# Performance work log

Measured on AMD Instinct MI355X. Metric: run time of the kernel, lower is better.

## Reference

```python
import jax, jax.numpy as jnp
import numpy as np

B = 1024
S_OUT, S_IN, D_IN = 30, 17, 3
H = 4
DKQ_I, DV_I, HID_I, OUT_I = 6, 8, 256, 64
DKQ_O, DV_O, HID_O = 64, 64, 1024
OUT_O = 36 * S_OUT  # 1080


def _mha(x, wq, bq, wk, bk, wv, bv, dkq):
    """Vectorized multi-head self-attention over all heads at once.
    x: [..., P, d_in]; wq/wk: [H, d_in, dkq]; wv: [H, d_in, dv].
    Returns context [..., H, P, dv] (matches torch stack+permute ordering)."""
    q = jnp.einsum('...pd,hdk->...hpk', x, wq) + bq[:, None, :]
    k = jnp.einsum('...pd,hdk->...hpk', x, wk) + bk[:, None, :]
    v = jnp.einsum('...pd,hdv->...hpv', x, wv) + bv[:, None, :]
    scores = jnp.einsum('...hpk,...hqk->...hpq', q, k) / jnp.sqrt(jnp.asarray(dkq, x.dtype))
    attn = jax.nn.softmax(scores, axis=-1)
    return jnp.einsum('...hpq,...hqv->...hpv', attn, v)


def _ml(ctx, w1, b1, w2, b2):
    """MultiHeadLinearLayer: per-head fc1+tanh (shared weights), concat heads, fc2.
    ctx: [..., H, P, dv] -> [..., out]."""
    lead = ctx.shape[:-3]
    flat = ctx.reshape(*lead, H, -1)            # [..., H, P*dv]
    h = jnp.tanh(flat @ w1 + b1)                # [..., H, hidden]
    h = h.reshape(*lead, -1)                    # [..., H*hidden]
    return h @ w2 + b2


def setup_inputs() -> dict:
    key = jax.random.key(0)
    ks = iter(jax.random.split(key, 32))
    n = lambda shape, s=0.05: jax.random.normal(next(ks), shape, dtype=jnp.float32) * s
    inp = {
        'x': jax.random.normal(next(ks), (B, S_OUT, S_IN, D_IN), dtype=jnp.float32),
        # inner multi-head attention (4 heads, stacked weights)
        'iwq': n((H, D_IN, DKQ_I)), 'ibq': n((H, DKQ_I)),
        'iwk': n((H, D_IN, DKQ_I)), 'ibk': n((H, DKQ_I)),
        'iwv': n((H, D_IN, DV_I)),  'ibv': n((H, DV_I)),
        # inner MultiHeadLinearLayer
        'iw1': n((S_IN * DV_I, HID_I)), 'ib1': n((HID_I,)),
        'iw2': n((H * HID_I, OUT_I)),   'ib2': n((OUT_I,)),
        # outer multi-head attention
        'owq': n((H, OUT_I, DKQ_O)), 'obq': n((H, DKQ_O)),
        'owk': n((H, OUT_I, DKQ_O)), 'obk': n((H, DKQ_O)),
        'owv': n((H, OUT_I, DV_O)),  'obv': n((H, DV_O)),
        # outer MultiHeadLinearLayer
        'ow1': n((S_OUT * DV_O, HID_O)), 'ob1': n((HID_O,)),
        'ow2': n((H * HID_O, OUT_O)),    'ob2': n((OUT_O,)),
    }
    return inp


def reference(x, iwq, ibq, iwk, ibk, iwv, ibv, iw1, ib1, iw2, ib2,
              owq, obq, owk, obk, owv, obv, ow1, ob1, ow2, ob2):
    b = x.shape[0]
    # Inner attention applied to all 30 outer positions at once (replaces python loop)
    ctx_i = _mha(x, iwq, ibq, iwk, ibk, iwv, ibv, DKQ_I)      # [B,30,H,17,8]
    seq = _ml(ctx_i, iw1, ib1, iw2, ib2)                       # [B,30,64]
    # Outer attention over the 30-step sequence
    ctx_o = _mha(seq, owq, obq, owk, obk, owv, obv, DKQ_O)     # [B,H,30,64]
    out = _ml(ctx_o, ow1, ob1, ow2, ob2)                       # [B,1080]
    return out.reshape(b, S_OUT, 12, 3)
```

## Files before the change

### kernel.cpp

```cpp
#include <hip/hip_runtime.h>


typedef _Float16 f16x8 __attribute__((ext_vector_type(8)));
typedef _Float16 f16x4 __attribute__((ext_vector_type(4)));
typedef float    f32x4 __attribute__((ext_vector_type(4)));
typedef float    f32x16 __attribute__((ext_vector_type(16)));

union F16x8u { f16x8 v; f16x4 q[2]; };

__device__ inline float tanh_fast(float x) {
    float ax = fabsf(x);
    float e  = __expf(2.0f * ax);
    float r  = 1.0f - 2.0f / (e + 1.0f);
    return copysignf(r, x);
}

__device__ inline f32x16 zero16() {
    f32x16 z;
    #pragma unroll
    for (int i = 0; i < 16; i++) z[i] = 0.f;
    return z;
}

__device__ inline void tcast_tile(
    const float* __restrict__ W, _Float16* __restrict__ Wt,
    int tileIdx, int nkx, int K, int N, int Kpad,
    _Float16 (*tile)[65], int t)
{
    const int kx = tileIdx % nkx, ny = tileIdx / nkx;
    const int k0 = kx * 64, n0 = ny * 64;
    for (int i = t; i < 4096; i += 256) {
        const int r = i >> 6, c = i & 63;
        const int k = k0 + r, n = n0 + c;
        float v = (k < K && n < N) ? W[(size_t)k * N + n] : 0.f;
        tile[c][r] = (_Float16)v;
    }
    __syncthreads();
    for (int i = t; i < 4096; i += 256) {
        const int r = i >> 6, c = i & 63;
        Wt[(size_t)(n0 + r) * Kpad + k0 + c] = tile[r][c];
    }
}

__global__ __launch_bounds__(256) void k_prep_all(
    const float* __restrict__ iwq, const float* __restrict__ ibq,
    const float* __restrict__ iwk, const float* __restrict__ ibk,
    const float* __restrict__ iwv, const float* __restrict__ ibv,
    const float* __restrict__ iw1, const float* __restrict__ iw2,
    const float* __restrict__ ow1, const float* __restrict__ ow2,
    const float* __restrict__ owq, const float* __restrict__ owk,
    const float* __restrict__ owv,
    _Float16* __restrict__ wqf, _Float16* __restrict__ wkf,
    _Float16* __restrict__ wvf,
    _Float16* __restrict__ iw1t, _Float16* __restrict__ iw2t,
    _Float16* __restrict__ ow1t, _Float16* __restrict__ ow2t,
    _Float16* __restrict__ owqt, _Float16* __restrict__ owkt,
    _Float16* __restrict__ owvt)
{
    __shared__ _Float16 tile[64][65];
    const int b = blockIdx.x, t = threadIdx.x;
    if (b == 0) {
        const float SC = 0.40824829046386307f;
        for (int i = t; i < 512; i += 256) {
            const int lanev = i >> 3, jj = i & 7;
            const int n = lanev & 31, grp = lanev >> 5;
            const int h = n >> 3, dk = n & 7;
            float q = 0.f, k = 0.f, v = 0.f;
            if (!grp) {
                if (jj < 3) {
                    if (dk < 6) { q = iwq[h*18 + jj*6 + dk] * SC; k = iwk[h*18 + jj*6 + dk]; }
                    v = iwv[h*24 + jj*8 + dk];
                } else if (jj == 3) {
                    if (dk < 6) { q = ibq[h*6 + dk] * SC; k = ibk[h*6 + dk]; }
                    v = ibv[h*8 + dk];
                }
            }
            wqf[i] = (_Float16)q; wkf[i] = (_Float16)k; wvf[i] = (_Float16)v;
        }
    } else if (b < 161) {
        const int idx = (b - 1) * 256 + t;
        if (idx < 40960) {
            const int n = idx / 160, kp = idx - n * 160;
            const int dv = kp / 20, p = kp - dv * 20;
            float v = (p < 17) ? iw1[(p*8 + dv) * 256 + n] : 0.f;
            iw1t[n * 160 + kp] = (_Float16)v;
        }
    } else if (b < 177) {
        tcast_tile(iw2, iw2t, b - 161, 16, 1024, 64, 1024, tile, t);
    } else if (b < 657) {
        tcast_tile(ow1, ow1t, b - 177, 30, 1920, 1024, 1920, tile, t);
    } else if (b < 1745) {
        tcast_tile(ow2, ow2t, b - 657, 64, 4096, 1080, 4096, tile, t);
    } else {
        const int s = b - 1745;
        const int mat = s >> 6, rem = s & 63;
        const int h = rem >> 4, blk = rem & 15;
        const int idx = blk * 256 + t;
        const int n = idx >> 6, k = idx & 63;
        const float* W = (mat == 0) ? owq : (mat == 1) ? owk : owv;
        _Float16* Wt   = (mat == 0) ? owqt : (mat == 1) ? owkt : owvt;
        Wt[h * 4096 + n * 64 + k] = (_Float16)W[h * 4096 + k * 64 + n];
    }
}

__global__ __launch_bounds__(256, 3) void k_inner_attn_mfma(
    const float* __restrict__ x,
    const _Float16* __restrict__ wqf, const _Float16* __restrict__ wkf,
    const _Float16* __restrict__ wvf,
    _Float16* __restrict__ flat)
{
    __shared__ __align__(16) _Float16 lds[4][5248];
    const int t = threadIdx.x, lane = t & 63, w = t >> 6;
    const int l31 = lane & 31, grp = lane >> 5;
    const int bs = blockIdx.x * 4 + w;
    _Float16* kq  = &lds[w][0];
    _Float16* qq  = &lds[w][1152];
    _Float16* vt  = &lds[w][2304];
    _Float16* pf  = &lds[w][3456];
    _Float16* fo2 = &lds[w][4608];

    f16x8 xf;
    #pragma unroll
    for (int i = 0; i < 8; i++) xf[i] = (_Float16)0.f;
    if (grp == 0 && l31 < 17) {
        const float* xr = x + (size_t)bs * 51 + l31 * 3;
        xf[0] = (_Float16)xr[0];
        xf[1] = (_Float16)xr[1];
        xf[2] = (_Float16)xr[2];
        xf[3] = (_Float16)1.0f;
    }
    const f16x8 wq8 = *(const f16x8*)&wqf[lane * 8];
    const f16x8 wk8 = *(const f16x8*)&wkf[lane * 8];
    const f16x8 wv8 = *(const f16x8*)&wvf[lane * 8];

    f32x16 kt = __builtin_amdgcn_mfma_f32_32x32x16_f16(wk8, xf, zero16(), 0, 0, 0);
    f32x16 qt = __builtin_amdgcn_mfma_f32_32x32x16_f16(wq8, xf, zero16(), 0, 0, 0);
    f32x16 vv = __builtin_amdgcn_mfma_f32_32x32x16_f16(xf, wv8, zero16(), 0, 0, 0);

    #pragma unroll
    for (int qd = 0; qd < 4; qd++) {
        const int base = 8 * qd + 4 * grp;
        f16x4 a, b, c;
        #pragma unroll
        for (int i = 0; i < 4; i++) {
            a[i] = (_Float16)kt[4*qd + i];
            b[i] = (_Float16)qt[4*qd + i];
            c[i] = (_Float16)vv[4*qd + i];
        }
        *(f16x4*)&kq[l31 * 36 + base] = a;
        *(f16x4*)&qq[l31 * 36 + base] = b;
        *(f16x4*)&vt[l31 * 36 + base] = c;
    }

    #pragma unroll
    for (int h = 0; h < 4; h++) {
        F16x8u ka, qb;
        #pragma unroll
        for (int i = 0; i < 8; i++) { ka.v[i] = (_Float16)0.f; qb.v[i] = (_Float16)0.f; }
        if (grp == 0) {
            ka.q[0] = *(const f16x4*)&kq[l31 * 36 + h * 8];
            ka.q[1] = *(const f16x4*)&kq[l31 * 36 + h * 8 + 4];
            qb.q[0] = *(const f16x4*)&qq[l31 * 36 + h * 8];
            qb.q[1] = *(const f16x4*)&qq[l31 * 36 + h * 8 + 4];
        }
        f32x16 s = __builtin_amdgcn_mfma_f32_32x32x16_f16(ka.v, qb.v, zero16(), 0, 0, 0);

        float mx = -1e30f;
        #pragma unroll
        for (int r = 0; r < 16; r++) {
            const bool val = (r < 8) || (r == 8 && grp == 0);
            if (val) mx = fmaxf(mx, s[r]);
        }
        mx = fmaxf(mx, __shfl_xor(mx, 32));
        float e[16], sum = 0.f;
        #pragma unroll
        for (int r = 0; r < 16; r++) {
            const bool val = (r < 8) || (r == 8 && grp == 0);
            e[r] = val ? __expf(s[r] - mx) : 0.f;
            sum += e[r];
        }
        sum += __shfl_xor(sum, 32);
        const float inv = __builtin_amdgcn_rcpf(sum);
        #pragma unroll
        for (int qd = 0; qd < 4; qd++) {
            f16x4 pk;
            #pragma unroll
            for (int i = 0; i < 4; i++) pk[i] = (_Float16)(e[4*qd + i] * inv);
            *(f16x4*)&pf[l31 * 36 + 8 * qd + 4 * grp] = pk;
        }

        F16x8u pa1, pa2, vb1, vb2;
        pa1.q[0] = *(const f16x4*)&pf[l31 * 36 + grp * 8];
        pa1.q[1] = *(const f16x4*)&pf[l31 * 36 + grp * 8 + 4];
        pa2.q[0] = *(const f16x4*)&pf[l31 * 36 + 16 + grp * 8];
        pa2.q[1] = *(const f16x4*)&pf[l31 * 36 + 16 + grp * 8 + 4];
        const int vr = (h * 8 + (l31 & 7)) * 36;
        vb1.q[0] = *(const f16x4*)&vt[vr + grp * 8];
        vb1.q[1] = *(const f16x4*)&vt[vr + grp * 8 + 4];
        vb2.q[0] = *(const f16x4*)&vt[vr + 16 + grp * 8];
        vb2.q[1] = *(const f16x4*)&vt[vr + 16 + grp * 8 + 4];
        f32x16 c = __builtin_amdgcn_mfma_f32_32x32x16_f16(pa1.v, vb1.v, zero16(), 0, 0, 0);
        c = __builtin_amdgcn_mfma_f32_32x32x16_f16(pa2.v, vb2.v, c, 0, 0, 0);

        if (l31 < 8) {
            #pragma unroll
            for (int qd = 0; qd < 4; qd++) {
                const int jb = 8 * qd + 4 * grp;
                if (jb < 20) {
                    f16x4 ck;
                    #pragma unroll
                    for (int i = 0; i < 4; i++) ck[i] = (_Float16)c[4*qd + i];
                    *(f16x4*)&fo2[h * 160 + l31 * 20 + jb] = ck;
                }
            }
        }
    }

    _Float16* fg = flat + (size_t)bs * 640;
    *(f16x8*)&fg[lane * 8] = *(const f16x8*)&fo2[lane * 8];
    if (lane < 16)
        *(f16x8*)&fg[512 + lane * 8] = *(const f16x8*)&fo2[512 + lane * 8];
}

__global__ __launch_bounds__(256) void k_inner_ml_mfma(
    const _Float16* __restrict__ flat,
    const _Float16* __restrict__ iw1t,
    const _Float16* __restrict__ iw2t,
    const float* __restrict__ ib1, const float* __restrict__ ib2,
    float* __restrict__ seq)
{
    __shared__ __align__(16) _Float16 h1l[32][1032];
    float* red = (float*)&h1l[0][0];
    const int t = threadIdx.x, lane = t & 63, w = t >> 6;
    const int q = lane >> 4, ml = lane & 15;
    const int m0  = blockIdx.x * 128;
    const int bs0 = blockIdx.x * 32;

    for (int p = 0; p < 2; p++) {
        f32x4 acc[4][4];
        #pragma unroll
        for (int mi = 0; mi < 4; mi++)
            #pragma unroll
            for (int ni = 0; ni < 4; ni++) acc[mi][ni] = (f32x4){0.f,0.f,0.f,0.f};
        for (int ks = 0; ks < 5; ks++) {
            const int k = ks * 32 + q * 8;
            f16x8 a[4], b[4];
            #pragma unroll
            for (int mi = 0; mi < 4; mi++)
                a[mi] = *(const f16x8*)&flat[(size_t)(m0 + p*64 + mi*16 + ml) * 160 + k];
            #pragma unroll
            for (int ni = 0; ni < 4; ni++)
                b[ni] = *(const f16x8*)&iw1t[(size_t)(w*64 + ni*16 + ml) * 160 + k];
            #pragma unroll
            for (int mi = 0; mi < 4; mi++)
                #pragma unroll
                for (int ni = 0; ni < 4; ni++)
                    acc[mi][ni] = __builtin_amdgcn_mfma_f32_16x16x32_f16(a[mi], b[ni], acc[mi][ni], 0, 0, 0);
        }
        #pragma unroll
        for (int mi = 0; mi < 4; mi++)
            #pragma unroll
            for (int ni = 0; ni < 4; ni++)
                #pragma unroll
                for (int r = 0; r < 4; r++) {
                    const int row = p*64 + mi*16 + q*4 + r;
                    const int col = w*64 + ni*16 + ml;
                    const int bs_l = row >> 2, h = row & 3;
                    h1l[bs_l][h*256 + col] = (_Float16)tanh_fast(acc[mi][ni][r] + ib1[col]);
                }
    }
    __syncthreads();

    f32x4 a2[2][4];
    #pragma unroll
    for (int mi = 0; mi < 2; mi++)
        #pragma unroll
        for (int ni = 0; ni < 4; ni++) a2[mi][ni] = (f32x4){0.f,0.f,0.f,0.f};
    for (int ks = 0; ks < 8; ks++) {
        const int k = w * 256 + ks * 32 + q * 8;
        f16x8 a[2], b[4];
        #pragma unroll
        for (int mi = 0; mi < 2; mi++)
            a[mi] = *(const f16x8*)&h1l[mi*16 + ml][k];
        #pragma unroll
        for (int ni = 0; ni < 4; ni++)
            b[ni] = *(const f16x8*)&iw2t[(size_t)(ni*16 + ml) * 1024 + k];
        #pragma unroll
        for (int mi = 0; mi < 2; mi++)
            #pragma unroll
            for (int ni = 0; ni < 4; ni++)
                a2[mi][ni] = __builtin_amdgcn_mfma_f32_16x16x32_f16(a[mi], b[ni], a2[mi][ni], 0, 0, 0);
    }
    __syncthreads();
    #pragma unroll
    for (int mi = 0; mi < 2; mi++)
        #pragma unroll
        for (int ni = 0; ni < 4; ni++)
            #pragma unroll
            for (int r = 0; r < 4; r++) {
                const int row = mi*16 + q*4 + r;
                const int col = ni*16 + ml;
                red[(size_t)w*2048 + row*64 + col] = a2[mi][ni][r];
            }
    __syncthreads();
    for (int i = t; i < 2048; i += 256) {
        const int row = i >> 6, col = i & 63;
        float s = red[i] + red[2048 + i] + red[4096 + i] + red[6144 + i] + ib2[col];
        seq[(size_t)(bs0 + row) * 64 + col] = s;
    }
}

__device__ inline void oa_proj_rows(
    const _Float16 (*seqf)[72], const _Float16* __restrict__ wt,
    const float* __restrict__ bias, _Float16 (*dst)[72], int q, int ml)
{
    f32x4 acc[2][4];
    #pragma unroll
    for (int mi = 0; mi < 2; mi++)
        #pragma unroll
        for (int ni = 0; ni < 4; ni++) acc[mi][ni] = (f32x4){0.f,0.f,0.f,0.f};
    #pragma unroll
    for (int k0 = 0; k0 < 64; k0 += 32) {
        f16x8 a[2], bb[4];
        #pragma unroll
        for (int mi = 0; mi < 2; mi++) a[mi] = *(const f16x8*)&seqf[mi*16 + ml][k0 + q*8];
        #pragma unroll
        for (int ni = 0; ni < 4; ni++) bb[ni] = *(const f16x8*)&wt[(size_t)(ni*16 + ml)*64 + k0 + q*8];
        #pragma unroll
        for (int mi = 0; mi < 2; mi++)
            #pragma unroll
            for (int ni = 0; ni < 4; ni++)
                acc[mi][ni] = __builtin_amdgcn_mfma_f32_16x16x32_f16(a[mi], bb[ni], acc[mi][ni], 0, 0, 0);
    }
    #pragma unroll
    for (int ni = 0; ni < 4; ni++) {
        const float bi = bias[ni*16 + ml];
        #pragma unroll
        for (int mi = 0; mi < 2; mi++)
            #pragma unroll
            for (int r = 0; r < 4; r++)
                dst[mi*16 + q*4 + r][ni*16 + ml] = (_Float16)(acc[mi][ni][r] + bi);
    }
}

__device__ inline void oa_proj_t(
    const _Float16 (*seqf)[72], const _Float16* __restrict__ wt,
    const float* __restrict__ bias, _Float16 (*dstT)[40], int q, int ml)
{
    f32x4 acc[2][4];
    #pragma unroll
    for (int mi = 0; mi < 2; mi++)
        #pragma unroll
        for (int ni = 0; ni < 4; ni++) acc[mi][ni] = (f32x4){0.f,0.f,0.f,0.f};
    #pragma unroll
    for (int k0 = 0; k0 < 64; k0 += 32) {
        f16x8 a[2], bb[4];
        #pragma unroll
        for (int mi = 0; mi < 2; mi++) a[mi] = *(const f16x8*)&seqf[mi*16 + ml][k0 + q*8];
        #pragma unroll
        for (int ni = 0; ni < 4; ni++) bb[ni] = *(const f16x8*)&wt[(size_t)(ni*16 + ml)*64 + k0 + q*8];
        #pragma unroll
        for (int mi = 0; mi < 2; mi++)
            #pragma unroll
            for (int ni = 0; ni < 4; ni++)
                acc[mi][ni] = __builtin_amdgcn_mfma_f32_16x16x32_f16(a[mi], bb[ni], acc[mi][ni], 0, 0, 0);
    }
    #pragma unroll
    for (int ni = 0; ni < 4; ni++) {
        const float bi = bias[ni*16 + ml];
        #pragma unroll
        for (int mi = 0; mi < 2; mi++)
            #pragma unroll
            for (int r = 0; r < 4; r++)
                dstT[ni*16 + ml][mi*16 + q*4 + r] = (_Float16)(acc[mi][ni][r] + bi);
    }
}

__global__ __launch_bounds__(256) void k_outer_attn_mfma(
    const float* __restrict__ seq,
    const _Float16* __restrict__ owqt,
    const _Float16* __restrict__ owkt,
    const _Float16* __restrict__ owvt,
    const float* __restrict__ obq, const float* __restrict__ obk,
    const float* __restrict__ obv,
    _Float16* __restrict__ ctxo)
{
    __shared__ __align__(16) _Float16 seqf[32][72];
    __shared__ __align__(16) _Float16 qf[4][32][72];
    __shared__ __align__(16) _Float16 kf[4][32][72];
    __shared__ __align__(16) _Float16 vt[4][64][40];
    __shared__ __align__(16) _Float16 pf[4][32][40];
    const int t = threadIdx.x, lane = t & 63, w = t >> 6;
    const int q = lane >> 4, ml = lane & 15;
    const int b = blockIdx.x;

    const float* sb = seq + (size_t)b * 1920;
    for (int i = t; i < 2048; i += 256) {
        const int row = i >> 6, col = i & 63;
        seqf[row][col] = (_Float16)(row < 30 ? sb[row*64 + col] : 0.0f);
    }
    __syncthreads();

    oa_proj_rows(seqf, owqt + w*4096, obq + w*64, qf[w], q, ml);
    oa_proj_rows(seqf, owkt + w*4096, obk + w*64, kf[w], q, ml);
    oa_proj_t   (seqf, owvt + w*4096, obv + w*64, vt[w], q, ml);
    __syncthreads();

    f32x4 sc[2][2];
    #pragma unroll
    for (int mi = 0; mi < 2; mi++)
        #pragma unroll
        for (int ni = 0; ni < 2; ni++) sc[mi][ni] = (f32x4){0.f,0.f,0.f,0.f};
    #pragma unroll
    for (int k0 = 0; k0 < 64; k0 += 32) {
        f16x8 aq[2], bk[2];
        #pragma unroll
        for (int mi = 0; mi < 2; mi++) aq[mi] = *(const f16x8*)&qf[w][mi*16 + ml][k0 + q*8];
        #pragma unroll
        for (int ni = 0; ni < 2; ni++) bk[ni] = *(const f16x8*)&kf[w][ni*16 + ml][k0 + q*8];
        #pragma unroll
        for (int mi = 0; mi < 2; mi++)
            #pragma unroll
            for (int ni = 0; ni < 2; ni++)
                sc[mi][ni] = __builtin_amdgcn_mfma_f32_16x16x32_f16(aq[mi], bk[ni], sc[mi][ni], 0, 0, 0);
    }

    const bool maskhi = (ml >= 14);
    #pragma unroll
    for (int mi = 0; mi < 2; mi++) {
        #pragma unroll
        for (int r = 0; r < 4; r++) {
            const float s0 = sc[mi][0][r] * 0.125f;
            const float s1 = maskhi ? -1e30f : sc[mi][1][r] * 0.125f;
            float mx = fmaxf(s0, s1);
            #pragma unroll
            for (int off = 1; off < 16; off <<= 1) mx = fmaxf(mx, __shfl_xor(mx, off, 64));
            const float e0 = __expf(s0 - mx);
            const float e1 = __expf(s1 - mx);
            float sm = e0 + e1;
            #pragma unroll
            for (int off = 1; off < 16; off <<= 1) sm += __shfl_xor(sm, off, 64);
            const float inv = 1.0f / sm;
            pf[w][mi*16 + q*4 + r][ml]      = (_Float16)(e0 * inv);
            pf[w][mi*16 + q*4 + r][16 + ml] = (_Float16)(e1 * inv);
        }
    }
    __syncthreads();

    f16x8 ap[2], bv[4];
    #pragma unroll
    for (int mi = 0; mi < 2; mi++) ap[mi] = *(const f16x8*)&pf[w][mi*16 + ml][q*8];
    #pragma unroll
    for (int ni = 0; ni < 4; ni++) bv[ni] = *(const f16x8*)&vt[w][ni*16 + ml][q*8];
    f32x4 oa[2][4];
    #pragma unroll
    for (int mi = 0; mi < 2; mi++)
        #pragma unroll
        for (int ni = 0; ni < 4; ni++) {
            oa[mi][ni] = (f32x4){0.f,0.f,0.f,0.f};
            oa[mi][ni] = __builtin_amdgcn_mfma_f32_16x16x32_f16(ap[mi], bv[ni], oa[mi][ni], 0, 0, 0);
        }

    _Float16* co = ctxo + (size_t)(b*4 + w) * 1920;
    #pragma unroll
    for (int mi = 0; mi < 2; mi++)
        #pragma unroll
        for (int r = 0; r < 4; r++) {
            const int row = mi*16 + q*4 + r;
            if (row < 30) {
                #pragma unroll
                for (int ni = 0; ni < 4; ni++)
                    co[row*64 + ni*16 + ml] = (_Float16)oa[mi][ni][r];
            }
        }
}

__global__ __launch_bounds__(128) void k_outer_fc1_mfma(
    const _Float16* __restrict__ ctxo,
    const _Float16* __restrict__ ow1t,
    const float* __restrict__ ob1,
    _Float16* __restrict__ hout)
{
    __shared__ float red[2][32][65];
    const int t = threadIdx.x, lane = t & 63, w = t >> 6;
    const int q = lane >> 4, ml = lane & 15;
    const int M0 = (blockIdx.x >> 4) * 32;
    const int N0 = (blockIdx.x & 15) * 64;
    const int kk0 = w * 960 + q * 8;
    f32x4 acc[2][4];
    #pragma unroll
    for (int mi = 0; mi < 2; mi++)
        #pragma unroll
        for (int ni = 0; ni < 4; ni++) acc[mi][ni] = (f32x4){0.f,0.f,0.f,0.f};
    f16x8 a[2][2], b[2][4];
    #pragma unroll
    for (int mi = 0; mi < 2; mi++)
        a[0][mi] = *(const f16x8*)&ctxo[(size_t)(M0 + mi*16 + ml) * 1920 + kk0];
    #pragma unroll
    for (int ni = 0; ni < 4; ni++)
        b[0][ni] = *(const f16x8*)&ow1t[(size_t)(N0 + ni*16 + ml) * 1920 + kk0];
    #pragma unroll
    for (int ks = 0; ks < 30; ks++) {
        const int cur = ks & 1, nxt = cur ^ 1;
        if (ks < 29) {
            const int kn = kk0 + (ks + 1) * 32;
            #pragma unroll
            for (int mi = 0; mi < 2; mi++)
                a[nxt][mi] = *(const f16x8*)&ctxo[(size_t)(M0 + mi*16 + ml) * 1920 + kn];
            #pragma unroll
            for (int ni = 0; ni < 4; ni++)
                b[nxt][ni] = *(const f16x8*)&ow1t[(size_t)(N0 + ni*16 + ml) * 1920 + kn];
        }
        #pragma unroll
        for (int mi = 0; mi < 2; mi++)
            #pragma unroll
            for (int ni = 0; ni < 4; ni++)
                acc[mi][ni] = __builtin_amdgcn_mfma_f32_16x16x32_f16(a[cur][mi], b[cur][ni], acc[mi][ni], 0, 0, 0);
    }
    #pragma unroll
    for (int mi = 0; mi < 2; mi++)
        #pragma unroll
        for (int ni = 0; ni < 4; ni++)
            #pragma unroll
            for (int r = 0; r < 4; r++)
                red[w][mi*16 + q*4 + r][ni*16 + ml] = acc[mi][ni][r];
    __syncthreads();
    for (int i = t; i < 2048; i += 128) {
        const int row = i >> 6, col = i & 63;
        const float s = red[0][row][col] + red[1][row][col] + ob1[N0 + col];
        hout[(size_t)(M0 + row) * 1024 + N0 + col] = (_Float16)tanh_fast(s);
    }
}

__global__ __launch_bounds__(256) void k_outer_fc2_mfma(
    const _Float16* __restrict__ hout,
    const _Float16* __restrict__ ow2t,
    float* __restrict__ part)
{
    __shared__ float red[4][32][65];
    const int t = threadIdx.x, lane = t & 63, w = t >> 6;
    const int q = lane >> 4, ml = lane & 15;
    const int bid = blockIdx.x;
    const int kc = bid & 3;
    const int rest = bid >> 2;
    const int M0 = (rest / 17) * 32;
    const int N0 = (rest % 17) * 64;
    const int kk0 = kc * 1024 + w * 256 + q * 8;
    f32x4 acc[2][4];
    #pragma unroll
    for (int mi = 0; mi < 2; mi++)
        #pragma unroll
        for (int ni = 0; ni < 4; ni++) acc[mi][ni] = (f32x4){0.f,0.f,0.f,0.f};
    f16x8 a[2][2], b[2][4];
    #pragma unroll
    for (int mi = 0; mi < 2; mi++)
        a[0][mi] = *(const f16x8*)&hout[(size_t)(M0 + mi*16 + ml) * 4096 + kk0];
    #pragma unroll
    for (int ni = 0; ni < 4; ni++)
        b[0][ni] = *(const f16x8*)&ow2t[(size_t)(N0 + ni*16 + ml) * 4096 + kk0];
    #pragma unroll
    for (int ks = 0; ks < 8; ks++) {
        const int cur = ks & 1, nxt = cur ^ 1;
        if (ks < 7) {
            const int kn = kk0 + (ks + 1) * 32;
            #pragma unroll
            for (int mi = 0; mi < 2; mi++)
                a[nxt][mi] = *(const f16x8*)&hout[(size_t)(M0 + mi*16 + ml) * 4096 + kn];
            #pragma unroll
            for (int ni = 0; ni < 4; ni++)
                b[nxt][ni] = *(const f16x8*)&ow2t[(size_t)(N0 + ni*16 + ml) * 4096 + kn];
        }
        #pragma unroll
        for (int mi = 0; mi < 2; mi++)
            #pragma unroll
            for (int ni = 0; ni < 4; ni++)
                acc[mi][ni] = __builtin_amdgcn_mfma_f32_16x16x32_f16(a[cur][mi], b[cur][ni], acc[mi][ni], 0, 0, 0);
    }
    #pragma unroll
    for (int mi = 0; mi < 2; mi++)
        #pragma unroll
        for (int ni = 0; ni < 4; ni++)
            #pragma unroll
            for (int r = 0; r < 4; r++)
                red[w][mi*16 + q*4 + r][ni*16 + ml] = acc[mi][ni][r];
    __syncthreads();
    for (int i = t; i < 2048; i += 256) {
        const int row = i >> 6, col = i & 63;
        const int n = N0 + col;
        if (n < 1080) {
            const float s = red[0][row][col] + red[1][row][col] + red[2][row][col] + red[3][row][col];
            part[(size_t)kc * 1105920 + (size_t)(M0 + row) * 1080 + n] = s;
        }
    }
}

__global__ __launch_bounds__(256) void k_fc2_reduce(
    const float* __restrict__ part, const float* __restrict__ ob2,
    float* __restrict__ out)
{
    const int idx = blockIdx.x * 256 + threadIdx.x;
    if (idx >= 1105920) return;
    const int n = idx % 1080;
    out[idx] = part[idx] + part[1105920 + idx] + part[2211840 + idx]
             + part[3317760 + idx] + ob2[n];
}

extern "C" void kernel_launch(void* const* d_in, const int* in_sizes, int n_in,
                              void* d_out, int out_size, void* d_ws, size_t ws_size,
                              hipStream_t stream) {
    const float* x   = (const float*)d_in[0];
    const float* iwq = (const float*)d_in[1];
    const float* ibq = (const float*)d_in[2];
    const float* iwk = (const float*)d_in[3];
    const float* ibk = (const float*)d_in[4];
    const float* iwv = (const float*)d_in[5];
    const float* ibv = (const float*)d_in[6];
    const float* iw1 = (const float*)d_in[7];
    const float* ib1 = (const float*)d_in[8];
    const float* iw2 = (const float*)d_in[9];
    const float* ib2 = (const float*)d_in[10];
    const float* owq = (const float*)d_in[11];
    const float* obq = (const float*)d_in[12];
    const float* owk = (const float*)d_in[13];
    const float* obk = (const float*)d_in[14];
    const float* owv = (const float*)d_in[15];
    const float* obv = (const float*)d_in[16];
    const float* ow1 = (const float*)d_in[17];
    const float* ob1 = (const float*)d_in[18];
    const float* ow2 = (const float*)d_in[19];
    const float* ob2 = (const float*)d_in[20];

    char* ws = (char*)d_ws;
    _Float16* iw1t   = (_Float16*)(ws + 0);
    _Float16* wqf    = (_Float16*)(ws + 98304);
    _Float16* wkf    = (_Float16*)(ws + 99328);
    _Float16* wvf    = (_Float16*)(ws + 100352);
    _Float16* iw2t   = (_Float16*)(ws + 163840);
    _Float16* ow1t   = (_Float16*)(ws + 294912);
    _Float16* ow2t   = (_Float16*)(ws + 4227072);
    _Float16* flat   = (_Float16*)(ws + 13139968);
    float*    seq    = (float*)   (ws + 52461568);
    _Float16* owqt   = (_Float16*)(ws + 60325888);
    _Float16* owkt   = (_Float16*)(ws + 60358656);
    _Float16* owvt   = (_Float16*)(ws + 60391424);
    _Float16* ctxo   = (_Float16*)(ws + 13139968);
    float*    part   = (float*)   (ws + 13139968);
    _Float16* houtb  = (_Float16*)(ws + 40000000);
    float*    out    = (float*)d_out;

    k_prep_all       <<<dim3(1937), dim3(256), 0, stream>>>(
        iwq, ibq, iwk, ibk, iwv, ibv, iw1, iw2, ow1, ow2, owq, owk, owv,
        wqf, wkf, wvf, iw1t, iw2t, ow1t, ow2t, owqt, owkt, owvt);
    k_inner_attn_mfma<<<dim3(7680), dim3(256), 0, stream>>>(x, wqf, wkf, wvf, flat);
    k_inner_ml_mfma  <<<dim3(960),  dim3(256), 0, stream>>>(flat, iw1t, iw2t, ib1, ib2, seq);
    k_outer_attn_mfma<<<dim3(1024), dim3(256), 0, stream>>>(seq, owqt, owkt, owvt, obq, obk, obv, ctxo);
    k_outer_fc1_mfma <<<dim3(2048), dim3(128), 0, stream>>>(ctxo, ow1t, ob1, houtb);
    k_outer_fc2_mfma <<<dim3(2176), dim3(256), 0, stream>>>(houtb, ow2t, part);
    k_fc2_reduce     <<<dim3(4320), dim3(256), 0, stream>>>(part, ob2, out);
}
```

Before: 363.5 us.

## Split outer fc1 K dimension across blocks with separate reduce kernel

The outer fc1 GEMM now splits K=1920 into three chunks across blocks and four waves per block (256 threads), writing fp16 partial sums to a workspace. A new reduce kernel sums the three partials, adds the bias and applies tanh. This raises parallelism and shortens the serial K loop per wave (5 steps instead of 30), at the cost of extra partial-sum traffic, an extra launch, and fp16 rounding of the partials.

Measured after the change: 371.1 us. 1.02x slower.

```diff
diff --git a/kernel.cpp b/kernel.cpp
--- a/kernel.cpp
+++ b/kernel.cpp
@@ -475,18 +475,20 @@
         }
 }
 
-__global__ __launch_bounds__(128) void k_outer_fc1_mfma(
+__global__ __launch_bounds__(256) void k_outer_fc1_mfma(
     const _Float16* __restrict__ ctxo,
     const _Float16* __restrict__ ow1t,
-    const float* __restrict__ ob1,
-    _Float16* __restrict__ hout)
-{
-    __shared__ float red[2][32][65];
+    _Float16* __restrict__ part1)
+{
+    __shared__ float red[4][32][65];
     const int t = threadIdx.x, lane = t & 63, w = t >> 6;
     const int q = lane >> 4, ml = lane & 15;
-    const int M0 = (blockIdx.x >> 4) * 32;
-    const int N0 = (blockIdx.x & 15) * 64;
-    const int kk0 = w * 960 + q * 8;
+    const int bid = blockIdx.x;
+    const int kc = bid % 3;
+    const int rest = bid / 3;
+    const int M0 = (rest >> 4) * 32;
+    const int N0 = (rest & 15) * 64;
+    const int kk0 = kc * 640 + w * 160 + q * 8;
     f32x4 acc[2][4];
     #pragma unroll
     for (int mi = 0; mi < 2; mi++)
@@ -500,9 +502,9 @@
     for (int ni = 0; ni < 4; ni++)
         b[0][ni] = *(const f16x8*)&ow1t[(size_t)(N0 + ni*16 + ml) * 1920 + kk0];
     #pragma unroll
-    for (int ks = 0; ks < 30; ks++) {
+    for (int ks = 0; ks < 5; ks++) {
         const int cur = ks & 1, nxt = cur ^ 1;
-        if (ks < 29) {
+        if (ks < 4) {
             const int kn = kk0 + (ks + 1) * 32;
             #pragma unroll
             for (int mi = 0; mi < 2; mi++)
@@ -525,11 +527,29 @@
             for (int r = 0; r < 4; r++)
                 red[w][mi*16 + q*4 + r][ni*16 + ml] = acc[mi][ni][r];
     __syncthreads();
-    for (int i = t; i < 2048; i += 128) {
+    for (int i = t; i < 2048; i += 256) {
         const int row = i >> 6, col = i & 63;
-        const float s = red[0][row][col] + red[1][row][col] + ob1[N0 + col];
-        hout[(size_t)(M0 + row) * 1024 + N0 + col] = (_Float16)tanh_fast(s);
-    }
+        const float s = red[0][row][col] + red[1][row][col] + red[2][row][col] + red[3][row][col];
+        part1[(size_t)kc * 4194304 + (size_t)(M0 + row) * 1024 + N0 + col] = (_Float16)s;
+    }
+}
+
+__global__ __launch_bounds__(256) void k_fc1_reduce(
+    const _Float16* __restrict__ part1, const float* __restrict__ ob1,
+    _Float16* __restrict__ hout)
+{
+    const int i8 = (blockIdx.x * 256 + threadIdx.x) * 8;
+    const int col = i8 & 1023;
+    const f16x8 p0 = *(const f16x8*)&part1[i8];
+    const f16x8 p1 = *(const f16x8*)&part1[4194304 + i8];
+    const f16x8 p2 = *(const f16x8*)&part1[8388608 + i8];
+    f16x8 o;
+    #pragma unroll
+    for (int j = 0; j < 8; j++) {
+        const float s = (float)p0[j] + (float)p1[j] + (float)p2[j] + ob1[col + j];
+        o[j] = (_Float16)tanh_fast(s);
+    }
+    *(f16x8*)&hout[i8] = o;
 }
 
 __global__ __launch_bounds__(256) void k_outer_fc2_mfma(
@@ -644,8 +664,9 @@
     _Float16* owkt   = (_Float16*)(ws + 60358656);
     _Float16* owvt   = (_Float16*)(ws + 60391424);
     _Float16* ctxo   = (_Float16*)(ws + 13139968);
-    float*    part   = (float*)   (ws + 13139968);
-    _Float16* houtb  = (_Float16*)(ws + 40000000);
+    float*    part2  = (float*)   (ws + 13139968);
+    _Float16* part1  = (_Float16*)(ws + 37257216);
+    _Float16* houtb  = (_Float16*)(ws + 62423040);
     float*    out    = (float*)d_out;
 
     k_prep_all       <<<dim3(1937), dim3(256), 0, stream>>>(
@@ -654,7 +675,8 @@
     k_inner_attn_mfma<<<dim3(7680), dim3(256), 0, stream>>>(x, wqf, wkf, wvf, flat);
     k_inner_ml_mfma  <<<dim3(960),  dim3(256), 0, stream>>>(flat, iw1t, iw2t, ib1, ib2, seq);
     k_outer_attn_mfma<<<dim3(1024), dim3(256), 0, stream>>>(seq, owqt, owkt, owvt, obq, obk, obv, ctxo);
-    k_outer_fc1_mfma <<<dim3(2048), dim3(128), 0, stream>>>(ctxo, ow1t, ob1, houtb);
-    k_outer_fc2_mfma <<<dim3(2176), dim3(256), 0, stream>>>(houtb, ow2t, part);
-    k_fc2_reduce     <<<dim3(4320), dim3(256), 0, stream>>>(part, ob2, out);
-}
+    k_outer_fc1_mfma <<<dim3(6144), dim3(256), 0, stream>>>(ctxo, ow1t, part1);
+    k_fc1_reduce     <<<dim3(2048), dim3(256), 0, stream>>>(part1, ob1, houtb);
+    k_outer_fc2_mfma <<<dim3(2176), dim3(256), 0, stream>>>(houtb, ow2t, part2);
+    k_fc2_reduce     <<<dim3(4320), dim3(256), 0, stream>>>(part2, ob2, out);
+}
```
